# Performance work log

Hardware: AMD Instinct MI355X
Metric: run time of the kernel (lower is better)

Reference implementation:

```python
import jax, jax.numpy as jnp
import numpy as np

NUM_REL = 3


def setup_inputs() -> dict:
    key = jax.random.key(0)
    ks = jax.random.split(key, 12)
    N, E, G = 400_000, 2_000_000, 40_000
    V, D, H, C = 1024, 64, 96, 8
    sc = lambda k, shape: (jax.random.normal(k, shape, jnp.float32) * 0.05)
    return {
        "tokens": jax.random.randint(ks[0], (N,), 0, V),
        "edge_index": jax.random.randint(ks[1], (2, E), 0, N),
        "edge_type": jax.random.randint(ks[2], (E,), 0, NUM_REL),
        "batch": jnp.sort(jax.random.randint(ks[3], (N,), 0, G)),
        "num_graphs": G,
        "emb": sc(ks[4], (V, D)),
        "W1": sc(ks[5], (NUM_REL, D, H)),
        "root1": sc(ks[6], (D, H)),
        "b1": jnp.zeros((H,), jnp.float32),
        "W2": sc(ks[7], (NUM_REL, H, H)),
        "root2": sc(ks[8], (H, H)),
        "b2": jnp.zeros((H,), jnp.float32),
        "linW": sc(ks[9], (H, C)),
        "linb": jnp.zeros((C,), jnp.float32),
    }


def rgcn_layer(x, src, dst, etype, W, root, bias):
    # PyG RGCNConv with default aggr='mean': per-relation mean over incoming
    # edges, transformed by the relation weight, plus root transform and bias.
    N, Din = x.shape
    seg = dst * NUM_REL + etype  # combined (node, relation) segment id
    msgs = x[src]  # [E, Din] irregular gather
    sums = jax.ops.segment_sum(msgs, seg, num_segments=N * NUM_REL)
    sums = sums.reshape(N, NUM_REL, Din)
    cnt = jax.ops.segment_sum(jnp.ones_like(etype, dtype=x.dtype), seg,
                              num_segments=N * NUM_REL).reshape(N, NUM_REL, 1)
    mean = sums / jnp.maximum(cnt, 1.0)
    return jnp.einsum("nrd,rdh->nh", mean, W) + x @ root + bias


def reference(tokens, edge_index, edge_type, batch, num_graphs,
              emb, W1, root1, b1, W2, root2, b2, linW, linb):
    src, dst = edge_index[0], edge_index[1]
    x = emb[tokens]  # [N, D]
    x = jax.nn.relu(rgcn_layer(x, src, dst, edge_type, W1, root1, b1))
    # dropout(p=0.2) is identity in eval mode
    x = jax.nn.relu(rgcn_layer(x, src, dst, edge_type, W2, root2, b2))
    gsum = jax.ops.segment_sum(x, batch, num_segments=num_graphs)
    gcnt = jax.ops.segment_sum(jnp.ones((x.shape[0], 1), x.dtype), batch,
                               num_segments=num_graphs)
    pooled = gsum / jnp.maximum(gcnt, 1.0)  # global_mean_pool
    return pooled @ linW + linb
```

## Files before the change

kernel.cpp:

```cpp
#include <hip/hip_runtime.h>


#define NREL 3
#define DD 64
#define HH 96
#define CC 8
#define TM 16
#define KK 384

typedef __attribute__((ext_vector_type(8))) short bf16x8;
typedef __attribute__((ext_vector_type(4))) short s16x4;
typedef __attribute__((ext_vector_type(4))) float f32x4;

__device__ __forceinline__ unsigned short f2bf(float x) {
    unsigned u = __float_as_uint(x);
    unsigned r = (u + 0x7fffu + ((u >> 16) & 1u)) >> 16;
    return (unsigned short)r;
}
__device__ __forceinline__ float bf2f(unsigned short h) {
    return __uint_as_float(((unsigned)h) << 16);
}

__global__ __launch_bounds__(256) void count_k(const int* __restrict__ dstv,
                                               const int* __restrict__ et, int E,
                                               int* __restrict__ cnt) {
    int e = blockIdx.x * 256 + threadIdx.x;
    if (e < E) atomicAdd(&cnt[dstv[e] * NREL + et[e]], 1);
}

__global__ __launch_bounds__(256) void scan_blk_k(const int* __restrict__ in, int S,
                                                  int* __restrict__ out,
                                                  int* __restrict__ bsum) {
    __shared__ int vals[1024];
    __shared__ int tsum[256];
    int base = blockIdx.x * 1024;
    for (int i = threadIdx.x; i < 1024; i += 256) {
        int g = base + i;
        vals[i] = (g < S) ? in[g] : 0;
    }
    __syncthreads();
    int t = threadIdx.x;
    int a0 = vals[t * 4], a1 = vals[t * 4 + 1], a2 = vals[t * 4 + 2], a3 = vals[t * 4 + 3];
    int s = a0 + a1 + a2 + a3;
    tsum[t] = s;
    __syncthreads();
    for (int off = 1; off < 256; off <<= 1) {
        int v = (t >= off) ? tsum[t - off] : 0;
        __syncthreads();
        tsum[t] += v;
        __syncthreads();
    }
    int excl = tsum[t] - s;
    int g = base + t * 4;
    if (g     < S) out[g]     = excl;
    if (g + 1 < S) out[g + 1] = excl + a0;
    if (g + 2 < S) out[g + 2] = excl + a0 + a1;
    if (g + 3 < S) out[g + 3] = excl + a0 + a1 + a2;
    if (t == 255) bsum[blockIdx.x] = tsum[255];
}

__global__ __launch_bounds__(256) void scan_top_k(int* __restrict__ bsum, int nb) {
    __shared__ int ts[256];
    int t = threadIdx.x;
    int loc[8];
    int s = 0;
    #pragma unroll
    for (int j = 0; j < 8; ++j) {
        int g = t * 8 + j;
        loc[j] = (g < nb) ? bsum[g] : 0;
        s += loc[j];
    }
    ts[t] = s;
    __syncthreads();
    for (int off = 1; off < 256; off <<= 1) {
        int v = (t >= off) ? ts[t - off] : 0;
        __syncthreads();
        ts[t] += v;
        __syncthreads();
    }
    int excl = ts[t] - s;
    #pragma unroll
    for (int j = 0; j < 8; ++j) {
        int g = t * 8 + j;
        if (g < nb) bsum[g] = excl;
        excl += loc[j];
    }
}

__global__ __launch_bounds__(256) void scan_add_k(int* __restrict__ out,
                                                  const int* __restrict__ bsum,
                                                  int S, int E) {
    int i = blockIdx.x * 256 + threadIdx.x;
    if (i < S) out[i] += bsum[i >> 10];
    else if (i == S) out[S] = E;
}

__global__ __launch_bounds__(256) void copy_k(const int* __restrict__ a,
                                              int* __restrict__ b, int n) {
    int i = blockIdx.x * 256 + threadIdx.x;
    if (i < n) b[i] = a[i];
}

__global__ __launch_bounds__(256) void fill_k(const int* __restrict__ srcv,
                                              const int* __restrict__ dstv,
                                              const int* __restrict__ et,
                                              const int* __restrict__ tokens, int E,
                                              int* __restrict__ cursor,
                                              int* __restrict__ ssrc,
                                              int* __restrict__ stok) {
    int e = blockIdx.x * 256 + threadIdx.x;
    if (e >= E) return;
    int s = srcv[e];
    int seg = dstv[e] * NREL + et[e];
    int pos = atomicAdd(&cursor[seg], 1);
    ssrc[pos] = s;
    stok[pos] = tokens[s];
}

__global__ __launch_bounds__(256) void gcnt_k(const int* __restrict__ batch, int N,
                                              float* __restrict__ gcnt) {
    int i = blockIdx.x * 256 + threadIdx.x;
    if (i < N) atomicAdd(&gcnt[batch[i]], 1.0f);
}

__global__ __launch_bounds__(256) void z1er_k(const float* __restrict__ emb,
                                              const float* __restrict__ W1,
                                              const float* __restrict__ root1,
                                              const float* __restrict__ b1,
                                              int V, float* __restrict__ z1,
                                              float* __restrict__ er1) {
    int idx = blockIdx.x * 256 + threadIdx.x;
    int tot = V * 4 * HH;
    if (idx >= tot) return;
    int v = idx / (4 * HH);
    int j = idx - v * 4 * HH;
    int r = j / HH;
    int h = j - r * HH;
    const float* ev = emb + (size_t)v * DD;
    float s = 0.f;
    if (r < NREL) {
        const float* w = W1 + ((size_t)r * DD) * HH + h;
        #pragma unroll 8
        for (int d = 0; d < DD; ++d) s += ev[d] * w[(size_t)d * HH];
        z1[((size_t)v * NREL + r) * HH + h] = s;
    } else {
        const float* w = root1 + h;
        #pragma unroll 8
        for (int d = 0; d < DD; ++d) s += ev[d] * w[(size_t)d * HH];
        er1[(size_t)v * HH + h] = s + b1[h];
    }
}

__global__ __launch_bounds__(256) void catwT_k(const float* __restrict__ W2,
                                               const float* __restrict__ root2,
                                               short* __restrict__ WTh,
                                               short* __restrict__ WTl) {
    int idx = blockIdx.x * 256 + threadIdx.x;
    const int tot = HH * KK;
    if (idx >= tot) return;
    int h = idx / KK;
    int K = idx - h * KK;
    float v = (K < NREL * HH) ? W2[(size_t)K * HH + h]
                              : root2[(size_t)(K - NREL * HH) * HH + h];
    unsigned short hi = f2bf(v);
    float res = v - bf2f(hi);
    unsigned short lo = f2bf(res);
    WTh[(size_t)h * KK + K] = (short)hi;
    WTl[(size_t)h * KK + K] = (short)lo;
}

__global__ __launch_bounds__(256) void l1_k(const int* __restrict__ rowptr,
                                            const int* __restrict__ stok,
                                            const int* __restrict__ tokens,
                                            const float* __restrict__ z1,
                                            const float* __restrict__ er1,
                                            unsigned short* __restrict__ h1h,
                                            unsigned short* __restrict__ h1l, int N) {
    int idx = blockIdx.x * 256 + threadIdx.x;
    if (idx >= N * 24) return;
    int n = idx / 24;
    int q = idx - n * 24;
    int h0 = q * 4;
    float4 acc = *reinterpret_cast<const float4*>(er1 + (size_t)tokens[n] * HH + h0);
    int base = n * NREL;
    for (int r = 0; r < NREL; ++r) {
        int b = rowptr[base + r], e2 = rowptr[base + r + 1];
        float sx = 0.f, sy = 0.f, sz = 0.f, sw = 0.f;
        for (int i = b; i < e2; ++i) {
            int tok = stok[i];
            const float4 z = *reinterpret_cast<const float4*>(
                z1 + ((size_t)tok * NREL + r) * HH + h0);
            sx += z.x; sy += z.y; sz += z.z; sw += z.w;
        }
        float rc = 1.0f / fmaxf((float)(e2 - b), 1.0f);
        acc.x += sx * rc; acc.y += sy * rc; acc.z += sz * rc; acc.w += sw * rc;
    }
    float o[4];
    o[0] = fmaxf(acc.x, 0.f); o[1] = fmaxf(acc.y, 0.f);
    o[2] = fmaxf(acc.z, 0.f); o[3] = fmaxf(acc.w, 0.f);
    s16x4 hv, lv;
    #pragma unroll
    for (int j = 0; j < 4; ++j) {
        unsigned short hb = f2bf(o[j]);
        float res = o[j] - bf2f(hb);
        hv[j] = (short)hb;
        lv[j] = (short)f2bf(res);
    }
    *reinterpret_cast<s16x4*>(&h1h[(size_t)n * HH + h0]) = hv;
    *reinterpret_cast<s16x4*>(&h1l[(size_t)n * HH + h0]) = lv;
}

__global__ __launch_bounds__(384, 8) void l2_k(const int* __restrict__ rowptr,
                                               const int* __restrict__ ssrc,
                                               const unsigned short* __restrict__ h1h,
                                               const unsigned short* __restrict__ h1l,
                                               const short* __restrict__ WTh,
                                               const short* __restrict__ WTl,
                                               const float* __restrict__ b2,
                                               const int* __restrict__ batch,
                                               float* __restrict__ gsum, int N) {
    __shared__ short Ah[TM][392];
    __shared__ short Al[TM][392];
    int n0 = blockIdx.x * TM;
    int t = threadIdx.x;
    {
        int i = t & 15;
        int c = t >> 4;
        int d0 = c * 16;
        int n = n0 + i;
        float acc[16];
        #pragma unroll
        for (int j = 0; j < 16; ++j) acc[j] = 0.f;
        if (n < N) {
            if (c < 18) {
                int r = c / 6;
                int k0 = (c - r * 6) * 16;
                int b = rowptr[n * NREL + r], e2 = rowptr[n * NREL + r + 1];
                for (int ii = b; ii < e2; ++ii) {
                    const unsigned short* hrow = h1h + (size_t)ssrc[ii] * HH + k0;
                    bf16x8 v0 = *reinterpret_cast<const bf16x8*>(hrow);
                    bf16x8 v1 = *reinterpret_cast<const bf16x8*>(hrow + 8);
                    #pragma unroll
                    for (int j = 0; j < 8; ++j) {
                        acc[j]     += bf2f((unsigned short)v0[j]);
                        acc[8 + j] += bf2f((unsigned short)v1[j]);
                    }
                }
                float rc = 1.0f / fmaxf((float)(e2 - b), 1.0f);
                #pragma unroll
                for (int j = 0; j < 16; ++j) acc[j] *= rc;
            } else {
                int k0 = (c - 18) * 16;
                const unsigned short* hrow = h1h + (size_t)n * HH + k0;
                const unsigned short* lrow = h1l + (size_t)n * HH + k0;
                bf16x8 v0 = *reinterpret_cast<const bf16x8*>(hrow);
                bf16x8 v1 = *reinterpret_cast<const bf16x8*>(hrow + 8);
                bf16x8 u0 = *reinterpret_cast<const bf16x8*>(lrow);
                bf16x8 u1 = *reinterpret_cast<const bf16x8*>(lrow + 8);
                #pragma unroll
                for (int j = 0; j < 8; ++j) {
                    acc[j]     = bf2f((unsigned short)v0[j]) + bf2f((unsigned short)u0[j]);
                    acc[8 + j] = bf2f((unsigned short)v1[j]) + bf2f((unsigned short)u1[j]);
                }
            }
        }
        #pragma unroll
        for (int w = 0; w < 2; ++w) {
            bf16x8 hv, lv;
            #pragma unroll
            for (int j = 0; j < 8; ++j) {
                float a = acc[w * 8 + j];
                unsigned short hb = f2bf(a);
                float res = a - bf2f(hb);
                unsigned short lb = f2bf(res);
                hv[j] = (short)hb;
                lv[j] = (short)lb;
            }
            *reinterpret_cast<bf16x8*>(&Ah[i][d0 + w * 8]) = hv;
            *reinterpret_cast<bf16x8*>(&Al[i][d0 + w * 8]) = lv;
        }
    }
    __syncthreads();
    int lane = t & 63;
    int w = t >> 6;
    int nb_ = w * 16;
    int r16 = lane & 15;
    int g = lane >> 4;

    float bi = b2[nb_ + r16];
    f32x4 acc = {bi, bi, bi, bi};

    const short* arow_h = &Ah[r16][8 * g];
    const short* arow_l = &Al[r16][8 * g];
    size_t wb = (size_t)(nb_ + r16) * KK + 8 * g;

    #pragma unroll
    for (int kk = 0; kk < KK / 32; ++kk) {
        int ko = kk * 32;
        bf16x8 ah = *reinterpret_cast<const bf16x8*>(arow_h + ko);
        bf16x8 al = *reinterpret_cast<const bf16x8*>(arow_l + ko);
        bf16x8 bh = *reinterpret_cast<const bf16x8*>(WTh + wb + ko);
        bf16x8 bl = *reinterpret_cast<const bf16x8*>(WTl + wb + ko);
        acc = __builtin_amdgcn_mfma_f32_16x16x32_bf16(ah, bh, acc, 0, 0, 0);
        acc = __builtin_amdgcn_mfma_f32_16x16x32_bf16(al, bh, acc, 0, 0, 0);
        acc = __builtin_amdgcn_mfma_f32_16x16x32_bf16(ah, bl, acc, 0, 0, 0);
    }
    #pragma unroll
    for (int r = 0; r < 4; ++r) {
        int node = n0 + g * 4 + r;
        if (node < N) {
            atomicAdd(gsum + (size_t)batch[node] * HH + nb_ + r16, fmaxf(acc[r], 0.f));
        }
    }
}

__global__ __launch_bounds__(256) void final_k(const float* __restrict__ gsum,
                                               const float* __restrict__ gcnt,
                                               const float* __restrict__ linW,
                                               const float* __restrict__ linb,
                                               float* __restrict__ out, int G) {
    int idx = blockIdx.x * 256 + threadIdx.x;
    if (idx >= G * CC) return;
    int g = idx / CC;
    int c = idx - g * CC;
    float rc = 1.0f / fmaxf(gcnt[g], 1.0f);
    const float* gs = gsum + (size_t)g * HH;
    float s = 0.f;
    #pragma unroll 8
    for (int h = 0; h < HH; ++h) s += gs[h] * linW[h * CC + c];
    out[idx] = s * rc + linb[c];
}

__global__ __launch_bounds__(256) void diag_k(float* __restrict__ out, int n, float v) {
    int i = blockIdx.x * 256 + threadIdx.x;
    if (i < n) out[i] = (i == 0) ? v : 0.f;
}

static inline int nblk(long long n) { return (int)((n + 255) / 256); }

extern "C" void kernel_launch(void* const* d_in, const int* in_sizes, int n_in,
                              void* d_out, int out_size, void* d_ws, size_t ws_size,
                              hipStream_t stream) {
    (void)n_in;
    const int* tokens = (const int*)d_in[0];
    const int* eidx   = (const int*)d_in[1];
    const int* etype  = (const int*)d_in[2];
    const int* batch  = (const int*)d_in[3];
    const float* emb   = (const float*)d_in[5];
    const float* W1    = (const float*)d_in[6];
    const float* root1 = (const float*)d_in[7];
    const float* b1    = (const float*)d_in[8];
    const float* W2    = (const float*)d_in[9];
    const float* root2 = (const float*)d_in[10];
    const float* b2v   = (const float*)d_in[11];
    const float* linW  = (const float*)d_in[12];
    const float* linb  = (const float*)d_in[13];
    float* out = (float*)d_out;

    const int N = in_sizes[0];
    const int E = in_sizes[2];
    const int V = in_sizes[5] / DD;
    const int G = out_size / CC;
    const int S = N * NREL;
    const int nb1 = (S + 1023) / 1024;

    const int* srcv = eidx;
    const int* dstv = eidx + E;

    auto align_up = [](size_t x) { return (x + 255) & ~(size_t)255; };
    size_t o_rowptr = 0;
    size_t o_cnt    = o_rowptr + align_up(((size_t)S + 1) * 4);
    size_t o_bsum   = o_cnt    + align_up((size_t)S * 4);
    size_t o_ssrc   = o_bsum   + align_up((size_t)2048 * 4);
    size_t o_stok   = o_ssrc   + align_up((size_t)E * 4);
    size_t o_z1     = o_stok   + align_up((size_t)E * 4);
    size_t o_er1    = o_z1     + align_up((size_t)V * NREL * HH * 4);
    size_t o_wth    = o_er1    + align_up((size_t)V * HH * 4);
    size_t o_wtl    = o_wth    + align_up((size_t)HH * KK * 2);
    size_t o_gsum   = o_wtl    + align_up((size_t)HH * KK * 2);
    size_t o_gcnt   = o_gsum   + align_up((size_t)G * HH * 4);
    size_t o_h1h    = o_gcnt   + align_up((size_t)G * 4);
    size_t o_h1l    = o_h1h    + align_up((size_t)N * HH * 2);
    size_t need     = o_h1l    + align_up((size_t)N * HH * 2);

    if (ws_size < need || nb1 > 2048) {
        diag_k<<<nblk(out_size), 256, 0, stream>>>(out, out_size, (float)ws_size);
        return;
    }

    char* ws = (char*)d_ws;
    int*   rowptr = (int*)  (ws + o_rowptr);
    int*   cnt    = (int*)  (ws + o_cnt);
    int*   bsum   = (int*)  (ws + o_bsum);
    int*   ssrc   = (int*)  (ws + o_ssrc);
    int*   stok   = (int*)  (ws + o_stok);
    float* z1     = (float*)(ws + o_z1);
    float* er1    = (float*)(ws + o_er1);
    short* WTh    = (short*)(ws + o_wth);
    short* WTl    = (short*)(ws + o_wtl);
    float* gsum   = (float*)(ws + o_gsum);
    float* gcntv  = (float*)(ws + o_gcnt);
    unsigned short* h1h = (unsigned short*)(ws + o_h1h);
    unsigned short* h1l = (unsigned short*)(ws + o_h1l);

    hipMemsetAsync(cnt, 0, (size_t)S * 4, stream);
    hipMemsetAsync(gsum, 0, (size_t)G * HH * 4, stream);
    hipMemsetAsync(gcntv, 0, (size_t)G * 4, stream);

    count_k<<<nblk(E), 256, 0, stream>>>(dstv, etype, E, cnt);
    scan_blk_k<<<nb1, 256, 0, stream>>>(cnt, S, rowptr, bsum);
    scan_top_k<<<1, 256, 0, stream>>>(bsum, nb1);
    scan_add_k<<<nblk((long long)S + 1), 256, 0, stream>>>(rowptr, bsum, S, E);
    copy_k<<<nblk(S), 256, 0, stream>>>(rowptr, cnt, S);
    fill_k<<<nblk(E), 256, 0, stream>>>(srcv, dstv, etype, tokens, E, cnt, ssrc, stok);
    z1er_k<<<nblk((long long)V * 4 * HH), 256, 0, stream>>>(emb, W1, root1, b1, V, z1, er1);
    catwT_k<<<nblk(HH * KK), 256, 0, stream>>>(W2, root2, WTh, WTl);
    gcnt_k<<<nblk(N), 256, 0, stream>>>(batch, N, gcntv);
    l1_k<<<nblk((long long)N * 24), 256, 0, stream>>>(rowptr, stok, tokens, z1, er1,
                                                      h1h, h1l, N);
    l2_k<<<(N + TM - 1) / TM, 384, 0, stream>>>(rowptr, ssrc, h1h, h1l, WTh, WTl, b2v,
                                                batch, gsum, N);
    final_k<<<nblk((long long)G * CC), 256, 0, stream>>>(gsum, gcntv, linW, linb, out, G);
}
```

Before: 0.9998 ms.

## Edge-parallel aggregation with LDS atomics in both RGCN layer kernels

Both layer kernels now process a tile of 16 destination nodes per block. Instead of one thread walking a node's variable-length edge list, the block spreads (edge, 16-column chunk) jobs across its threads, finds each edge's segment with a binary search over a cached rowptr slice, and accumulates the gathered rows into shared memory with float atomics. The goal is to remove load imbalance and serialised per-thread loops caused by variable in-degree. The cost is shared-memory atomic contention, extra LDS zeroing, an added sync, and lower occupancy from the larger fp32 shared buffers. Float atomics also make the summation order nondeterministic.

After: 2.479 ms. +147.9%, slower.

```diff
diff --git a/kernel.cpp b/kernel.cpp
--- a/kernel.cpp
+++ b/kernel.cpp
@@ -169,48 +169,84 @@
     WTl[(size_t)h * KK + K] = (short)lo;
 }
 
-__global__ __launch_bounds__(256) void l1_k(const int* __restrict__ rowptr,
-                                            const int* __restrict__ stok,
-                                            const int* __restrict__ tokens,
-                                            const float* __restrict__ z1,
-                                            const float* __restrict__ er1,
-                                            unsigned short* __restrict__ h1h,
-                                            unsigned short* __restrict__ h1l, int N) {
-    int idx = blockIdx.x * 256 + threadIdx.x;
-    if (idx >= N * 24) return;
-    int n = idx / 24;
-    int q = idx - n * 24;
-    int h0 = q * 4;
-    float4 acc = *reinterpret_cast<const float4*>(er1 + (size_t)tokens[n] * HH + h0);
-    int base = n * NREL;
-    for (int r = 0; r < NREL; ++r) {
-        int b = rowptr[base + r], e2 = rowptr[base + r + 1];
-        float sx = 0.f, sy = 0.f, sz = 0.f, sw = 0.f;
-        for (int i = b; i < e2; ++i) {
-            int tok = stok[i];
-            const float4 z = *reinterpret_cast<const float4*>(
-                z1 + ((size_t)tok * NREL + r) * HH + h0);
-            sx += z.x; sy += z.y; sz += z.z; sw += z.w;
-        }
-        float rc = 1.0f / fmaxf((float)(e2 - b), 1.0f);
-        acc.x += sx * rc; acc.y += sy * rc; acc.z += sz * rc; acc.w += sw * rc;
-    }
-    float o[4];
-    o[0] = fmaxf(acc.x, 0.f); o[1] = fmaxf(acc.y, 0.f);
-    o[2] = fmaxf(acc.z, 0.f); o[3] = fmaxf(acc.w, 0.f);
-    s16x4 hv, lv;
-    #pragma unroll
-    for (int j = 0; j < 4; ++j) {
-        unsigned short hb = f2bf(o[j]);
-        float res = o[j] - bf2f(hb);
-        hv[j] = (short)hb;
-        lv[j] = (short)f2bf(res);
-    }
-    *reinterpret_cast<s16x4*>(&h1h[(size_t)n * HH + h0]) = hv;
-    *reinterpret_cast<s16x4*>(&h1l[(size_t)n * HH + h0]) = lv;
-}
-
-__global__ __launch_bounds__(384, 8) void l2_k(const int* __restrict__ rowptr,
+__device__ __forceinline__ int segsearch(const int* rp, int ge) {
+    int lo = 0, hi = 47;
+    while (lo < hi) {
+        int mid = (lo + hi) >> 1;
+        if (rp[mid + 1] <= ge) lo = mid + 1; else hi = mid;
+    }
+    return lo;
+}
+
+__global__ __launch_bounds__(384, 7) void l1_k(const int* __restrict__ rowptr,
+                                               const int* __restrict__ stok,
+                                               const int* __restrict__ tokens,
+                                               const float* __restrict__ z1,
+                                               const float* __restrict__ er1,
+                                               unsigned short* __restrict__ h1h,
+                                               unsigned short* __restrict__ h1l,
+                                               int N) {
+    __shared__ float B1[TM][296];
+    __shared__ int rp[49];
+    int n0 = blockIdx.x * TM;
+    int t = threadIdx.x;
+    for (int j = t; j < TM * 296; j += 384) ((float*)B1)[j] = 0.f;
+    if (t < 49) {
+        int idx = n0 * NREL + t;
+        int mx = N * NREL;
+        rp[t] = rowptr[idx < mx ? idx : mx];
+    }
+    __syncthreads();
+    int e0 = rp[0];
+    int jobs = (rp[48] - e0) * 6;
+    for (int j = t; j < jobs; j += 384) {
+        int e = j / 6;
+        int c = j - e * 6;
+        int ge = e0 + e;
+        int s = segsearch(rp, ge);
+        int i = s / NREL;
+        int r = s - i * NREL;
+        const float* zr = z1 + ((size_t)stok[ge] * NREL + r) * HH + c * 16;
+        float* brow = &B1[i][r * HH + c * 16];
+        #pragma unroll
+        for (int jj = 0; jj < 16; jj += 4) {
+            const float4 v = *reinterpret_cast<const float4*>(zr + jj);
+            atomicAdd(brow + jj + 0, v.x);
+            atomicAdd(brow + jj + 1, v.y);
+            atomicAdd(brow + jj + 2, v.z);
+            atomicAdd(brow + jj + 3, v.w);
+        }
+    }
+    __syncthreads();
+    int i = t / 24;
+    int q = t - i * 24;
+    int n = n0 + i;
+    if (i < TM && n < N) {
+        const float4 ev = *reinterpret_cast<const float4*>(
+            er1 + (size_t)tokens[n] * HH + q * 4);
+        float a[4] = {ev.x, ev.y, ev.z, ev.w};
+        #pragma unroll
+        for (int r = 0; r < NREL; ++r) {
+            float deg = (float)(rp[i * NREL + r + 1] - rp[i * NREL + r]);
+            float rc = 1.0f / fmaxf(deg, 1.0f);
+            #pragma unroll
+            for (int jj = 0; jj < 4; ++jj) a[jj] += B1[i][r * HH + q * 4 + jj] * rc;
+        }
+        s16x4 hv, lv;
+        #pragma unroll
+        for (int jj = 0; jj < 4; ++jj) {
+            float o = fmaxf(a[jj], 0.f);
+            unsigned short hb = f2bf(o);
+            float res = o - bf2f(hb);
+            hv[jj] = (short)hb;
+            lv[jj] = (short)f2bf(res);
+        }
+        *reinterpret_cast<s16x4*>(&h1h[(size_t)n * HH + q * 4]) = hv;
+        *reinterpret_cast<s16x4*>(&h1l[(size_t)n * HH + q * 4]) = lv;
+    }
+}
+
+__global__ __launch_bounds__(384, 7) void l2_k(const int* __restrict__ rowptr,
                                                const int* __restrict__ ssrc,
                                                const unsigned short* __restrict__ h1h,
                                                const unsigned short* __restrict__ h1l,
@@ -219,65 +255,83 @@
                                                const float* __restrict__ b2,
                                                const int* __restrict__ batch,
                                                float* __restrict__ gsum, int N) {
-    __shared__ short Ah[TM][392];
-    __shared__ short Al[TM][392];
+    __shared__ float Af32[TM][392];
+    __shared__ int rp[49];
+    short* ab = (short*)&Af32[0][0];
     int n0 = blockIdx.x * TM;
     int t = threadIdx.x;
+    for (int j = t; j < TM * 392; j += 384) ((float*)Af32)[j] = 0.f;
+    if (t < 49) {
+        int idx = n0 * NREL + t;
+        int mx = N * NREL;
+        rp[t] = rowptr[idx < mx ? idx : mx];
+    }
+    __syncthreads();
+    int e0 = rp[0];
+    int jobs = (rp[48] - e0) * 6;
+    for (int j = t; j < jobs; j += 384) {
+        int e = j / 6;
+        int c = j - e * 6;
+        int ge = e0 + e;
+        int s = segsearch(rp, ge);
+        int i = s / NREL;
+        int r = s - i * NREL;
+        const unsigned short* hr = h1h + (size_t)ssrc[ge] * HH + c * 16;
+        bf16x8 v0 = *reinterpret_cast<const bf16x8*>(hr);
+        bf16x8 v1 = *reinterpret_cast<const bf16x8*>(hr + 8);
+        float* arow = &Af32[i][r * HH + c * 16];
+        #pragma unroll
+        for (int jj = 0; jj < 8; ++jj) {
+            atomicAdd(arow + jj,     bf2f((unsigned short)v0[jj]));
+            atomicAdd(arow + 8 + jj, bf2f((unsigned short)v1[jj]));
+        }
+    }
+    __syncthreads();
+    int i = t & 15;
+    int c2 = t >> 4;
+    int d0 = c2 * 16;
+    int n = n0 + i;
+    float a[16];
+    #pragma unroll
+    for (int jj = 0; jj < 16; ++jj) a[jj] = 0.f;
+    if (n < N) {
+        if (c2 < 18) {
+            int r = c2 / 6;
+            int k0 = (c2 - r * 6) * 16;
+            float deg = (float)(rp[i * NREL + r + 1] - rp[i * NREL + r]);
+            float rc = 1.0f / fmaxf(deg, 1.0f);
+            #pragma unroll
+            for (int jj = 0; jj < 16; ++jj) a[jj] = Af32[i][r * HH + k0 + jj] * rc;
+        } else {
+            int k0 = (c2 - 18) * 16;
+            const unsigned short* hr = h1h + (size_t)n * HH + k0;
+            const unsigned short* lr = h1l + (size_t)n * HH + k0;
+            bf16x8 v0 = *reinterpret_cast<const bf16x8*>(hr);
+            bf16x8 v1 = *reinterpret_cast<const bf16x8*>(hr + 8);
+            bf16x8 u0 = *reinterpret_cast<const bf16x8*>(lr);
+            bf16x8 u1 = *reinterpret_cast<const bf16x8*>(lr + 8);
+            #pragma unroll
+            for (int jj = 0; jj < 8; ++jj) {
+                a[jj]     = bf2f((unsigned short)v0[jj]) + bf2f((unsigned short)u0[jj]);
+                a[8 + jj] = bf2f((unsigned short)v1[jj]) + bf2f((unsigned short)u1[jj]);
+            }
+        }
+    }
+    __syncthreads();
     {
-        int i = t & 15;
-        int c = t >> 4;
-        int d0 = c * 16;
-        int n = n0 + i;
-        float acc[16];
-        #pragma unroll
-        for (int j = 0; j < 16; ++j) acc[j] = 0.f;
-        if (n < N) {
-            if (c < 18) {
-                int r = c / 6;
-                int k0 = (c - r * 6) * 16;
-                int b = rowptr[n * NREL + r], e2 = rowptr[n * NREL + r + 1];
-                for (int ii = b; ii < e2; ++ii) {
-                    const unsigned short* hrow = h1h + (size_t)ssrc[ii] * HH + k0;
-                    bf16x8 v0 = *reinterpret_cast<const bf16x8*>(hrow);
-                    bf16x8 v1 = *reinterpret_cast<const bf16x8*>(hrow + 8);
-                    #pragma unroll
-                    for (int j = 0; j < 8; ++j) {
-                        acc[j]     += bf2f((unsigned short)v0[j]);
-                        acc[8 + j] += bf2f((unsigned short)v1[j]);
-                    }
-                }
-                float rc = 1.0f / fmaxf((float)(e2 - b), 1.0f);
-                #pragma unroll
-                for (int j = 0; j < 16; ++j) acc[j] *= rc;
-            } else {
-                int k0 = (c - 18) * 16;
-                const unsigned short* hrow = h1h + (size_t)n * HH + k0;
-                const unsigned short* lrow = h1l + (size_t)n * HH + k0;
-                bf16x8 v0 = *reinterpret_cast<const bf16x8*>(hrow);
-                bf16x8 v1 = *reinterpret_cast<const bf16x8*>(hrow + 8);
-                bf16x8 u0 = *reinterpret_cast<const bf16x8*>(lrow);
-                bf16x8 u1 = *reinterpret_cast<const bf16x8*>(lrow + 8);
-                #pragma unroll
-                for (int j = 0; j < 8; ++j) {
-                    acc[j]     = bf2f((unsigned short)v0[j]) + bf2f((unsigned short)u0[j]);
-                    acc[8 + j] = bf2f((unsigned short)v1[j]) + bf2f((unsigned short)u1[j]);
-                }
-            }
-        }
+        bf16x8 hv, lv;
         #pragma unroll
         for (int w = 0; w < 2; ++w) {
-            bf16x8 hv, lv;
             #pragma unroll
-            for (int j = 0; j < 8; ++j) {
-                float a = acc[w * 8 + j];
-                unsigned short hb = f2bf(a);
-                float res = a - bf2f(hb);
-                unsigned short lb = f2bf(res);
-                hv[j] = (short)hb;
-                lv[j] = (short)lb;
+            for (int jj = 0; jj < 8; ++jj) {
+                float x = a[w * 8 + jj];
+                unsigned short hb = f2bf(x);
+                float res = x - bf2f(hb);
+                hv[jj] = (short)hb;
+                lv[jj] = (short)f2bf(res);
             }
-            *reinterpret_cast<bf16x8*>(&Ah[i][d0 + w * 8]) = hv;
-            *reinterpret_cast<bf16x8*>(&Al[i][d0 + w * 8]) = lv;
+            *reinterpret_cast<bf16x8*>(ab + i * 392 + d0 + w * 8) = hv;
+            *reinterpret_cast<bf16x8*>(ab + TM * 392 + i * 392 + d0 + w * 8) = lv;
         }
     }
     __syncthreads();
@@ -290,8 +344,8 @@
     float bi = b2[nb_ + r16];
     f32x4 acc = {bi, bi, bi, bi};
 
-    const short* arow_h = &Ah[r16][8 * g];
-    const short* arow_l = &Al[r16][8 * g];
+    const short* arow_h = ab + r16 * 392 + 8 * g;
+    const short* arow_l = ab + TM * 392 + r16 * 392 + 8 * g;
     size_t wb = (size_t)(nb_ + r16) * KK + 8 * g;
 
     #pragma unroll
@@ -416,8 +470,8 @@
     z1er_k<<<nblk((long long)V * 4 * HH), 256, 0, stream>>>(emb, W1, root1, b1, V, z1, er1);
     catwT_k<<<nblk(HH * KK), 256, 0, stream>>>(W2, root2, WTh, WTl);
     gcnt_k<<<nblk(N), 256, 0, stream>>>(batch, N, gcntv);
-    l1_k<<<nblk((long long)N * 24), 256, 0, stream>>>(rowptr, stok, tokens, z1, er1,
-                                                      h1h, h1l, N);
+    l1_k<<<(N + TM - 1) / TM, 384, 0, stream>>>(rowptr, stok, tokens, z1, er1,
+                                                h1h, h1l, N);
     l2_k<<<(N + TM - 1) / TM, 384, 0, stream>>>(rowptr, ssrc, h1h, h1l, WTh, WTl, b2v,
                                                 batch, gsum, N);
     final_k<<<nblk((long long)G * CC), 256, 0, stream>>>(gsum, gcntv, linW, linb, out, G);
```
